# Kernel optimization log

Hardware: AMD Instinct MI355X
Metric: run time of the kernel (lower is better)

The kernel has to match this reference:

```python
import jax, jax.numpy as jnp
import numpy as np

P_EPS = 1e-6            # nn.PairwiseDistance default eps
ALPHA = 0.25
STD_TARGET = 1.0
NUM_COMMUNITIES = 512   # C = number of unique community ids
BIG = 1e30              # masking value for hard-negative min


def setup_inputs() -> dict:
    key = jax.random.key(0)
    k1, k2, k3 = jax.random.split(key, 3)
    B, N, D, C = 1, 100000, 128, NUM_COMMUNITIES
    node_features = jax.random.normal(k1, (B, N, D), dtype=jnp.float32)
    # row 0: a permutation of node indices; row 1: community of that node.
    perm = jax.random.permutation(k2, N).astype(jnp.int32)
    comm_per_node = jnp.concatenate([
        jnp.arange(C, dtype=jnp.int32),  # guarantee every community appears
        jax.random.randint(k3, (N - C,), 0, C, dtype=jnp.int32),
    ])
    community_belong_list = jnp.stack([perm, comm_per_node[perm]])  # [2, N]
    return {"node_features": node_features, "community_belong_list": community_belong_list}


def reference(node_features, community_belong_list):
    B, N, D = node_features.shape
    C = NUM_COMMUNITIES
    dt = node_features.dtype

    # ---- _community_inverse_permute: invert row-0 permutation, reorder columns ----
    perm = community_belong_list[0]
    inv = jnp.zeros((N,), perm.dtype).at[perm].add(jnp.arange(N, dtype=perm.dtype))
    cbl = community_belong_list[:, inv]          # row0 == arange(N) after this
    comm = cbl[1]                                # [N] community id per node
    src = node_features[:, cbl[0], :]            # [B,N,D] gather (identity order)

    # ---- groupby sum / count -> community means ----
    comm_sum = jnp.zeros((B, C, D), dt).at[:, comm, :].add(src)        # [B,C,D]
    counts = jnp.zeros((C,), dt).at[comm].add(jnp.asarray(1.0, dt))   # [C]
    comm_mean = comm_sum / counts[None, :, None]                      # [B,C,D]

    # ---- cdist(node_features, comm_mean, p=2) -> [B,N,C] ----
    x2 = jnp.sum(node_features * node_features, -1)                   # [B,N]
    c2 = jnp.sum(comm_mean * comm_mean, -1)                           # [B,C]
    dots = jnp.einsum('bnd,bcd->bnc', node_features, comm_mean)
    distance = jnp.sqrt(jnp.maximum(x2[:, :, None] + c2[:, None, :] - 2.0 * dots, 0.0))

    # ---- leave-one-out community mean per node, positive distance ----
    cnt_pn = counts[comm]                                             # [N]
    cnt_m1 = jnp.maximum(cnt_pn - 1.0, 1.0)                           # [N]
    x_minus = jnp.where((cnt_pn == 1.0)[None, :, None], jnp.asarray(0.0, dt), src)
    loo_mean = (comm_sum[:, comm, :] - x_minus) / cnt_m1[None, :, None]
    pos_dist = jnp.sqrt(jnp.sum((loo_mean - src + P_EPS) ** 2, -1))   # [B,N]

    # ---- negatives: all communities except the node's own ----
    own = distance[:, jnp.arange(N), comm]                            # [B,N]
    mean_neg = (jnp.sum(distance, -1) - own) / (C - 1)                # [B,N]
    pos_mask = jnp.zeros((N, C), bool).at[jnp.arange(N), comm].set(True)
    hard_neg = jnp.min(jnp.where(pos_mask[None], jnp.asarray(BIG, dt), distance), -1)

    trip_mean = jnp.maximum(pos_dist - mean_neg + ALPHA, 0.0)
    trip_min = jnp.maximum(pos_dist - hard_neg + ALPHA, 0.0)

    # ---- groupby std (unbiased) per community per feature ----
    sq = jnp.zeros((B, C, D), dt).at[:, comm, :].add((src - comm_mean[:, comm, :]) ** 2)
    std = jnp.sqrt(sq / jnp.maximum(counts - 1.0, 1.0)[None, :, None])

    return (trip_mean.mean(), trip_min.mean(), ((std - STD_TARGET) ** 2).mean())
```

## Files before the change

### kernel.cpp

```cpp
#include <hip/hip_runtime.h>

#define NCOMM 512
#define DIM   128
#define ALPHA 0.25f
#define PEPS  1e-6f
#define BIGF  1e30f
#define TILE_C 16
#define NT    (NCOMM / TILE_C)

typedef __attribute__((ext_vector_type(8))) _Float16 f16x8;
typedef __attribute__((ext_vector_type(4))) float f32x4;

#define GLOAD_LDS16(g, l) __builtin_amdgcn_global_load_lds( \
    (const __attribute__((address_space(1))) void*)(g), \
    (__attribute__((address_space(3))) void*)(l), 16, 0, 0)


__global__ void k_prep(const int* __restrict__ cbl, int* __restrict__ comm,
                       int* __restrict__ counts, int N) {
    __shared__ int h[NCOMM];
    int t = threadIdx.x;
    h[t] = 0; h[t + 256] = 0;
    __syncthreads();
    int i = blockIdx.x * 256 + t;
    if (i < N) {
        int p = cbl[i];
        int c = cbl[N + i];
        comm[p] = c;
        atomicAdd(&h[c], 1);
    }
    __syncthreads();
    int v = h[t];        if (v) atomicAdd(&counts[t], v);
    v = h[t + 256];      if (v) atomicAdd(&counts[t + 256], v);
}

__global__ void k_scan(const int* __restrict__ counts, int* __restrict__ offsets,
                       int* __restrict__ cursor, float* __restrict__ countf) {
    __shared__ int sc[NCOMM];
    int t = threadIdx.x;
    int v0 = counts[t];
    sc[t] = v0;
    __syncthreads();
    for (int off = 1; off < NCOMM; off <<= 1) {
        int v = (t >= off) ? sc[t - off] : 0;
        __syncthreads();
        sc[t] += v;
        __syncthreads();
    }
    int excl = sc[t] - v0;
    offsets[t] = excl;
    cursor[t]  = excl;
    countf[t]  = (float)v0;
}

__global__ void k_sort(const int* __restrict__ comm, int* __restrict__ cursor,
                       int* __restrict__ sorted, int N) {
    __shared__ int h[NCOMM], hb[NCOMM];
    int t = threadIdx.x;
    h[t] = 0; h[t + 256] = 0;
    __syncthreads();
    int j0 = blockIdx.x * 1024 + t;
    int cs[4];
    #pragma unroll
    for (int q = 0; q < 4; ++q) {
        int j = j0 + q * 256;
        cs[q] = (j < N) ? comm[j] : -1;
        if (cs[q] >= 0) atomicAdd(&h[cs[q]], 1);
    }
    __syncthreads();
    int v = h[t];        if (v) hb[t] = atomicAdd(&cursor[t], v);
    v = h[t + 256];      if (v) hb[t + 256] = atomicAdd(&cursor[t + 256], v);
    __syncthreads();
    #pragma unroll
    for (int q = 0; q < 4; ++q) {
        int j = j0 + q * 256;
        if (cs[q] >= 0) {
            int p = atomicAdd(&hb[cs[q]], 1);
            sorted[p] = j;
        }
    }
}


__global__ void __launch_bounds__(256) k_stats(
        const float* __restrict__ NF,
        const int* __restrict__ sorted, const int* __restrict__ offsets,
        const int* __restrict__ counts,
        float* __restrict__ comm_sum,
        _Float16* __restrict__ CMh,
        float* __restrict__ c2, float* __restrict__ accum) {
    __shared__ int ridx[512];
    __shared__ float4 bufS[256], bufQ[256];
    int c = blockIdx.x, t = threadIdx.x;
    int d4 = t & 31, r = t >> 5;
    int cnt = counts[c], base = offsets[c];
    const float4* NF4 = (const float4*)NF;

    float4 s4 = make_float4(0.f, 0.f, 0.f, 0.f);
    float4 q4 = make_float4(0.f, 0.f, 0.f, 0.f);
    for (int chunk = 0; chunk < cnt; chunk += 512) {
        int m = min(cnt - chunk, 512);
        for (int i = t; i < m; i += 256) ridx[i] = sorted[base + chunk + i];
        __syncthreads();
        int i = r;
        for (; i + 24 < m; i += 32) {
            int a0 = ridx[i], a1 = ridx[i + 8], a2 = ridx[i + 16], a3 = ridx[i + 24];
            float4 v0 = NF4[(size_t)a0 * 32 + d4];
            float4 v1 = NF4[(size_t)a1 * 32 + d4];
            float4 v2 = NF4[(size_t)a2 * 32 + d4];
            float4 v3 = NF4[(size_t)a3 * 32 + d4];
            s4.x += v0.x; s4.y += v0.y; s4.z += v0.z; s4.w += v0.w;
            q4.x = fmaf(v0.x, v0.x, q4.x); q4.y = fmaf(v0.y, v0.y, q4.y);
            q4.z = fmaf(v0.z, v0.z, q4.z); q4.w = fmaf(v0.w, v0.w, q4.w);
            s4.x += v1.x; s4.y += v1.y; s4.z += v1.z; s4.w += v1.w;
            q4.x = fmaf(v1.x, v1.x, q4.x); q4.y = fmaf(v1.y, v1.y, q4.y);
            q4.z = fmaf(v1.z, v1.z, q4.z); q4.w = fmaf(v1.w, v1.w, q4.w);
            s4.x += v2.x; s4.y += v2.y; s4.z += v2.z; s4.w += v2.w;
            q4.x = fmaf(v2.x, v2.x, q4.x); q4.y = fmaf(v2.y, v2.y, q4.y);
            q4.z = fmaf(v2.z, v2.z, q4.z); q4.w = fmaf(v2.w, v2.w, q4.w);
            s4.x += v3.x; s4.y += v3.y; s4.z += v3.z; s4.w += v3.w;
            q4.x = fmaf(v3.x, v3.x, q4.x); q4.y = fmaf(v3.y, v3.y, q4.y);
            q4.z = fmaf(v3.z, v3.z, q4.z); q4.w = fmaf(v3.w, v3.w, q4.w);
        }
        for (; i < m; i += 8) {
            float4 v = NF4[(size_t)ridx[i] * 32 + d4];
            s4.x += v.x; s4.y += v.y; s4.z += v.z; s4.w += v.w;
            q4.x = fmaf(v.x, v.x, q4.x); q4.y = fmaf(v.y, v.y, q4.y);
            q4.z = fmaf(v.z, v.z, q4.z); q4.w = fmaf(v.w, v.w, q4.w);
        }
        __syncthreads();
    }
    bufS[t] = s4; bufQ[t] = q4;
    __syncthreads();
    if (t < 128) {
        float4 a = bufS[t], b = bufS[t + 128];
        a.x += b.x; a.y += b.y; a.z += b.z; a.w += b.w; bufS[t] = a;
        float4 e = bufQ[t], f = bufQ[t + 128];
        e.x += f.x; e.y += f.y; e.z += f.z; e.w += f.w; bufQ[t] = e;
    }
    __syncthreads();
    if (t < 64) {
        float4 a = bufS[t], b = bufS[t + 64];
        a.x += b.x; a.y += b.y; a.z += b.z; a.w += b.w; bufS[t] = a;
        float4 e = bufQ[t], f = bufQ[t + 64];
        e.x += f.x; e.y += f.y; e.z += f.z; e.w += f.w; bufQ[t] = e;
    }
    __syncthreads();
    if (t < 32) {
        float4 a = bufS[t], b = bufS[t + 32];
        a.x += b.x; a.y += b.y; a.z += b.z; a.w += b.w;
        float4 e = bufQ[t], f = bufQ[t + 32];
        e.x += f.x; e.y += f.y; e.z += f.z; e.w += f.w;
        float sarr[4] = {a.x, a.y, a.z, a.w};
        float qarr[4] = {e.x, e.y, e.z, e.w};
        float cf = (float)cnt;
        float mm = 0.f, ee = 0.f;
        #pragma unroll
        for (int k = 0; k < 4; ++k) {
            int d = t * 4 + k;
            float s = sarr[k];
            comm_sum[c * DIM + d] = s;
            float m = (cnt > 0) ? s / cf : 0.f;
            CMh[c * DIM + d] = (_Float16)m;
            float varn = fmaxf(fmaf(-cf * m, m, qarr[k]), 0.f);
            float stdv = sqrtf(varn / fmaxf(cf - 1.f, 1.f));
            float er = stdv - 1.f;
            mm = fmaf(m, m, mm);
            ee = fmaf(er, er, ee);
        }
        #pragma unroll
        for (int msk = 1; msk < 32; msk <<= 1) {
            mm += __shfl_xor(mm, msk);
            ee += __shfl_xor(ee, msk);
        }
        if (t == 0) {
            c2[c] = mm;
            atomicAdd(&accum[2], ee);
        }
    }
}


__global__ void __launch_bounds__(256, 4) k_main(
        const float* __restrict__ NF,
        const _Float16* __restrict__ CMh,
        const float* __restrict__ comm_sum,
        const float* __restrict__ c2g,
        const float* __restrict__ countf,
        const int* __restrict__ comm,
        float* __restrict__ accum, int N) {
    __shared__ _Float16 Bst[4][4][TILE_C * 64];
    __shared__ float c2s[NCOMM];
    __shared__ int   comms[128];
    __shared__ float x2sh[128];
    __shared__ float sums[128], mins[128];
    __shared__ float red[8];

    int tid = threadIdx.x;
    int w  = tid >> 6;
    int l  = tid & 63;
    int lr = l & 15;
    int lk = l >> 4;
    int n0 = blockIdx.x * 128;

    int off0 = ((l >> 3) << 7) + (((l & 7) ^ ((l >> 3) & 7)) << 3);
    const _Float16* gsrc = CMh + off0;
    auto stage = [&](int ss, int b) {
        const _Float16* g = gsrc + (size_t)(ss >> 1) * 2048 + (ss & 1) * 64;
        _Float16* lh = &Bst[w][b][0];
        GLOAD_LDS16(g,        lh);
        GLOAD_LDS16(g + 1024, lh + 512);
    };
    stage(0, 0); stage(1, 1); stage(2, 2);

    c2s[tid]       = c2g[tid];
    c2s[tid + 256] = c2g[tid + 256];
    if (tid < 128) {
        int gn = n0 + tid;
        comms[tid] = (gn < N) ? comm[gn] : -1;
    }

    f16x8 ah[2][4];
    #pragma unroll
    for (int mf = 0; mf < 2; ++mf) {
        int n = n0 + w * 32 + mf * 16 + lr;
        const float4* src = (const float4*)NF + (size_t)n * 32 + lk * 2;
        float p2 = 0.f;
        #pragma unroll
        for (int ks = 0; ks < 4; ++ks) {
            float4 v0 = make_float4(0.f, 0.f, 0.f, 0.f), v1 = v0;
            if (n < N) { v0 = src[ks * 8]; v1 = src[ks * 8 + 1]; }
            float fr[8] = {v0.x, v0.y, v0.z, v0.w, v1.x, v1.y, v1.z, v1.w};
            f16x8 hh;
            #pragma unroll
            for (int t = 0; t < 8; ++t) {
                hh[t] = (_Float16)fr[t];
                p2 = fmaf(fr[t], fr[t], p2);
            }
            ah[mf][ks] = hh;
        }
        p2 += __shfl_xor(p2, 16);
        p2 += __shfl_xor(p2, 32);
        if (lk == 0) x2sh[w * 32 + mf * 16 + lr] = -0.5f * p2;
    }
    __syncthreads();

    f32x4 x2v[2];
    int cnv[2][4];
    float sumv[2][4], minv[2][4];
    #pragma unroll
    for (int mf = 0; mf < 2; ++mf) {
        x2v[mf] = *(const f32x4*)&x2sh[w * 32 + mf * 16 + lk * 4];
        #pragma unroll
        for (int j = 0; j < 4; ++j) {
            cnv[mf][j] = comms[w * 32 + mf * 16 + lk * 4 + j];
            sumv[mf][j] = 0.f; minv[mf][j] = BIGF;
        }
    }

    for (int tt = 0; tt < NT; ++tt) {
        f32x4 acc0, acc1;
        {
            int ssn = 2 * tt + 3;
            if (ssn < 64) stage(ssn, ssn & 3);
            if (tt <= 30) { asm volatile("s_waitcnt vmcnt(6)" ::: "memory"); }
            else          { asm volatile("s_waitcnt vmcnt(2)" ::: "memory"); }
            const _Float16* bp = &Bst[w][(2 * tt) & 3][0];
            acc0 = x2v[0]; acc1 = x2v[1];
            #pragma unroll
            for (int ks2 = 0; ks2 < 2; ++ks2) {
                int ch = (ks2 * 4 + lk) ^ (lr & 7);
                f16x8 b = *(const f16x8*)&bp[(size_t)(lr * 64 + ch * 8)];
                acc0 = __builtin_amdgcn_mfma_f32_16x16x32_f16(ah[0][ks2], b, acc0, 0, 0, 0);
                acc1 = __builtin_amdgcn_mfma_f32_16x16x32_f16(ah[1][ks2], b, acc1, 0, 0, 0);
            }
        }
        {
            int ssn = 2 * tt + 4;
            if (ssn < 64) stage(ssn, ssn & 3);
            if (tt <= 29)      { asm volatile("s_waitcnt vmcnt(6)" ::: "memory"); }
            else if (tt == 30) { asm volatile("s_waitcnt vmcnt(4)" ::: "memory"); }
            else               { asm volatile("s_waitcnt vmcnt(0)" ::: "memory"); }
            const _Float16* bp = &Bst[w][(2 * tt + 1) & 3][0];
            #pragma unroll
            for (int ks2 = 0; ks2 < 2; ++ks2) {
                int ch = (ks2 * 4 + lk) ^ (lr & 7);
                f16x8 b = *(const f16x8*)&bp[(size_t)(lr * 64 + ch * 8)];
                acc0 = __builtin_amdgcn_mfma_f32_16x16x32_f16(ah[0][2 + ks2], b, acc0, 0, 0, 0);
                acc1 = __builtin_amdgcn_mfma_f32_16x16x32_f16(ah[1][2 + ks2], b, acc1, 0, 0, 0);
            }
            int ccol = tt * TILE_C + lr;
            float c2v = c2s[ccol];
            #pragma unroll
            for (int j = 0; j < 4; ++j) {
                float d2a = fmaf(-2.f, acc0[j], c2v);
                float da  = __builtin_amdgcn_sqrtf(fmaxf(d2a, 0.f));
                sumv[0][j] += da;
                minv[0][j] = fminf(minv[0][j], (cnv[0][j] == ccol) ? BIGF : da);
                float d2b = fmaf(-2.f, acc1[j], c2v);
                float db  = __builtin_amdgcn_sqrtf(fmaxf(d2b, 0.f));
                sumv[1][j] += db;
                minv[1][j] = fminf(minv[1][j], (cnv[1][j] == ccol) ? BIGF : db);
            }
        }
    }

    #pragma unroll
    for (int mf = 0; mf < 2; ++mf)
        #pragma unroll
        for (int j = 0; j < 4; ++j) {
            float sv = sumv[mf][j], mv = minv[mf][j];
            #pragma unroll
            for (int msk = 1; msk < 16; msk <<= 1) {
                sv += __shfl_xor(sv, msk);
                mv = fminf(mv, __shfl_xor(mv, msk));
            }
            if (lr == 0) {
                int idx = w * 32 + mf * 16 + lk * 4 + j;
                sums[idx] = sv; mins[idx] = mv;
            }
        }
    __syncthreads();

    float tmean = 0.f, tminv = 0.f;
    {
        int ln = tid >> 1, half = tid & 1;
        int n = n0 + ln;
        if (n < N) {
            int cnode = comms[ln];
            float cf  = countf[cnode];
            float cm1 = fmaxf(cf - 1.f, 1.f);
            float rs  = 1.f / cm1;
            bool single = (cf == 1.f);
            const float4* srow = (const float4*)NF + (size_t)n * 32 + half * 16;
            const float4* csum = (const float4*)(comm_sum + (size_t)cnode * DIM) + half * 16;
            float q = 0.f, dot = 0.f;
            #pragma unroll
            for (int m = 0; m < 16; ++m) {
                float4 sv = srow[m];
                float4 cs = csum[m];
                float4 xm = single ? make_float4(0.f, 0.f, 0.f, 0.f) : sv;
                float lx = (cs.x - xm.x) * rs - sv.x + PEPS;
                float ly = (cs.y - xm.y) * rs - sv.y + PEPS;
                float lz = (cs.z - xm.z) * rs - sv.z + PEPS;
                float lw = (cs.w - xm.w) * rs - sv.w + PEPS;
                q = fmaf(lx, lx, fmaf(ly, ly, fmaf(lz, lz, fmaf(lw, lw, q))));
                dot = fmaf(sv.x, cs.x, fmaf(sv.y, cs.y, fmaf(sv.z, cs.z, fmaf(sv.w, cs.w, dot))));
            }
            q   += __shfl_xor(q, 1);
            dot += __shfl_xor(dot, 1);
            if (half == 0) {
                float pos = sqrtf(q);
                float x2 = -2.f * x2sh[ln];
                float ownd2 = x2 + c2s[cnode] - 2.f * (dot / cf);
                float own = sqrtf(fmaxf(ownd2, 0.f));
                float mean_neg = (sums[ln] - own) * (1.f / (float)(NCOMM - 1));
                tmean = fmaxf(pos - mean_neg + ALPHA, 0.f);
                tminv = fmaxf(pos - mins[ln] + ALPHA, 0.f);
            }
        }
    }
    #pragma unroll
    for (int msk = 1; msk < 64; msk <<= 1) {
        tmean += __shfl_xor(tmean, msk);
        tminv += __shfl_xor(tminv, msk);
    }
    if ((tid & 63) == 0) { red[w * 2] = tmean; red[w * 2 + 1] = tminv; }
    __syncthreads();
    if (tid == 0) {
        atomicAdd(&accum[0], red[0] + red[2] + red[4] + red[6]);
        atomicAdd(&accum[1], red[1] + red[3] + red[5] + red[7]);
    }
}

__global__ void k_final(const float* __restrict__ accum, float* __restrict__ out, int N) {
    if (threadIdx.x == 0) {
        out[0] = accum[0] / (float)N;
        out[1] = accum[1] / (float)N;
        out[2] = accum[2] / (float)(NCOMM * DIM);
    }
}


extern "C" void kernel_launch(void* const* d_in, const int* in_sizes, int n_in,
                              void* d_out, int out_size, void* d_ws, size_t ws_size,
                              hipStream_t stream) {
    const float* NF  = (const float*)d_in[0];
    const int*   CBL = (const int*)d_in[1];
    int N = in_sizes[1] / 2;
    if (N <= 0) return;

    char* ws = (char*)d_ws;
    float* accum   = (float*)ws;
    int*   counts  = (int*)(ws + 16);
    int*   cursor  = (int*)(ws + 16 + 2048);
    int*   offsets = (int*)(ws + 16 + 2 * 2048);
    float* countf  = (float*)(ws + 16 + 3 * 2048);
    float* c2      = (float*)(ws + 16 + 4 * 2048);
    char* p = ws + 16 + 5 * 2048;
    int* comm   = (int*)p; p += (size_t)N * 4;
    int* sorted = (int*)p; p += (size_t)N * 4;
    float* comm_sum = (float*)p; p += (size_t)NCOMM * DIM * 4;
    _Float16* CMh = (_Float16*)p;

    hipMemsetAsync(d_ws, 0, 16 + 2048, stream);

    int nb = (N + 255) / 256;
    k_prep<<<nb, 256, 0, stream>>>(CBL, comm, counts, N);
    k_scan<<<1, NCOMM, 0, stream>>>(counts, offsets, cursor, countf);
    int nb4 = (N + 1023) / 1024;
    k_sort<<<nb4, 256, 0, stream>>>(comm, cursor, sorted, N);
    k_stats<<<NCOMM, 256, 0, stream>>>(NF, sorted, offsets, counts,
                                       comm_sum, CMh, c2, accum);
    int mb = (N + 127) / 128;
    k_main<<<mb, 256, 0, stream>>>(NF, CMh, comm_sum, c2, countf,
                                   comm, accum, N);
    k_final<<<1, 64, 0, stream>>>(accum, (float*)d_out, N);
}
```

Baseline: 120.8 us.

## Use 2 waves per block with 64 rows each to double B-tile reuse

Result: faster. 118.2 us (median of 2 runs) (-2.2%).

```diff
diff --git a/kernel.cpp b/kernel.cpp
--- a/kernel.cpp
+++ b/kernel.cpp
@@ -181,7 +181,7 @@
 }
 
 
-__global__ void __launch_bounds__(256, 4) k_main(
+__global__ void __launch_bounds__(128, 2) k_main(
         const float* __restrict__ NF,
         const _Float16* __restrict__ CMh,
         const float* __restrict__ comm_sum,
@@ -189,12 +189,12 @@
         const float* __restrict__ countf,
         const int* __restrict__ comm,
         float* __restrict__ accum, int N) {
-    __shared__ _Float16 Bst[4][4][TILE_C * 64];
+    __shared__ _Float16 Bst[2][4][TILE_C * 64];
     __shared__ float c2s[NCOMM];
     __shared__ int   comms[128];
     __shared__ float x2sh[128];
     __shared__ float sums[128], mins[128];
-    __shared__ float red[8];
+    __shared__ float red[4];
 
     int tid = threadIdx.x;
     int w  = tid >> 6;
@@ -214,16 +214,18 @@
     stage(0, 0); stage(1, 1); stage(2, 2);
 
     c2s[tid]       = c2g[tid];
+    c2s[tid + 128] = c2g[tid + 128];
     c2s[tid + 256] = c2g[tid + 256];
-    if (tid < 128) {
+    c2s[tid + 384] = c2g[tid + 384];
+    {
         int gn = n0 + tid;
         comms[tid] = (gn < N) ? comm[gn] : -1;
     }
 
-    f16x8 ah[2][4];
-    #pragma unroll
-    for (int mf = 0; mf < 2; ++mf) {
-        int n = n0 + w * 32 + mf * 16 + lr;
+    f16x8 ah[4][4];
+    #pragma unroll
+    for (int mf = 0; mf < 4; ++mf) {
+        int n = n0 + w * 64 + mf * 16 + lr;
         const float4* src = (const float4*)NF + (size_t)n * 32 + lk * 2;
         float p2 = 0.f;
         #pragma unroll
@@ -241,38 +243,40 @@
         }
         p2 += __shfl_xor(p2, 16);
         p2 += __shfl_xor(p2, 32);
-        if (lk == 0) x2sh[w * 32 + mf * 16 + lr] = -0.5f * p2;
-    }
-    __syncthreads();
-
-    f32x4 x2v[2];
-    int cnv[2][4];
-    float sumv[2][4], minv[2][4];
-    #pragma unroll
-    for (int mf = 0; mf < 2; ++mf) {
-        x2v[mf] = *(const f32x4*)&x2sh[w * 32 + mf * 16 + lk * 4];
+        if (lk == 0) x2sh[w * 64 + mf * 16 + lr] = -0.5f * p2;
+    }
+    __syncthreads();
+
+    f32x4 x2v[4];
+    int cnv[4][4];
+    float sumv[4][4], minv[4][4];
+    #pragma unroll
+    for (int mf = 0; mf < 4; ++mf) {
+        x2v[mf] = *(const f32x4*)&x2sh[w * 64 + mf * 16 + lk * 4];
         #pragma unroll
         for (int j = 0; j < 4; ++j) {
-            cnv[mf][j] = comms[w * 32 + mf * 16 + lk * 4 + j];
+            cnv[mf][j] = comms[w * 64 + mf * 16 + lk * 4 + j];
             sumv[mf][j] = 0.f; minv[mf][j] = BIGF;
         }
     }
 
     for (int tt = 0; tt < NT; ++tt) {
-        f32x4 acc0, acc1;
+        f32x4 acc0, acc1, acc2, acc3;
         {
             int ssn = 2 * tt + 3;
             if (ssn < 64) stage(ssn, ssn & 3);
             if (tt <= 30) { asm volatile("s_waitcnt vmcnt(6)" ::: "memory"); }
             else          { asm volatile("s_waitcnt vmcnt(2)" ::: "memory"); }
             const _Float16* bp = &Bst[w][(2 * tt) & 3][0];
-            acc0 = x2v[0]; acc1 = x2v[1];
+            acc0 = x2v[0]; acc1 = x2v[1]; acc2 = x2v[2]; acc3 = x2v[3];
             #pragma unroll
             for (int ks2 = 0; ks2 < 2; ++ks2) {
                 int ch = (ks2 * 4 + lk) ^ (lr & 7);
                 f16x8 b = *(const f16x8*)&bp[(size_t)(lr * 64 + ch * 8)];
                 acc0 = __builtin_amdgcn_mfma_f32_16x16x32_f16(ah[0][ks2], b, acc0, 0, 0, 0);
                 acc1 = __builtin_amdgcn_mfma_f32_16x16x32_f16(ah[1][ks2], b, acc1, 0, 0, 0);
+                acc2 = __builtin_amdgcn_mfma_f32_16x16x32_f16(ah[2][ks2], b, acc2, 0, 0, 0);
+                acc3 = __builtin_amdgcn_mfma_f32_16x16x32_f16(ah[3][ks2], b, acc3, 0, 0, 0);
             }
         }
         {
@@ -288,6 +292,8 @@
                 f16x8 b = *(const f16x8*)&bp[(size_t)(lr * 64 + ch * 8)];
                 acc0 = __builtin_amdgcn_mfma_f32_16x16x32_f16(ah[0][2 + ks2], b, acc0, 0, 0, 0);
                 acc1 = __builtin_amdgcn_mfma_f32_16x16x32_f16(ah[1][2 + ks2], b, acc1, 0, 0, 0);
+                acc2 = __builtin_amdgcn_mfma_f32_16x16x32_f16(ah[2][2 + ks2], b, acc2, 0, 0, 0);
+                acc3 = __builtin_amdgcn_mfma_f32_16x16x32_f16(ah[3][2 + ks2], b, acc3, 0, 0, 0);
             }
             int ccol = tt * TILE_C + lr;
             float c2v = c2s[ccol];
@@ -301,12 +307,20 @@
                 float db  = __builtin_amdgcn_sqrtf(fmaxf(d2b, 0.f));
                 sumv[1][j] += db;
                 minv[1][j] = fminf(minv[1][j], (cnv[1][j] == ccol) ? BIGF : db);
-            }
-        }
-    }
-
-    #pragma unroll
-    for (int mf = 0; mf < 2; ++mf)
+                float d2c = fmaf(-2.f, acc2[j], c2v);
+                float dc  = __builtin_amdgcn_sqrtf(fmaxf(d2c, 0.f));
+                sumv[2][j] += dc;
+                minv[2][j] = fminf(minv[2][j], (cnv[2][j] == ccol) ? BIGF : dc);
+                float d2d = fmaf(-2.f, acc3[j], c2v);
+                float dd  = __builtin_amdgcn_sqrtf(fmaxf(d2d, 0.f));
+                sumv[3][j] += dd;
+                minv[3][j] = fminf(minv[3][j], (cnv[3][j] == ccol) ? BIGF : dd);
+            }
+        }
+    }
+
+    #pragma unroll
+    for (int mf = 0; mf < 4; ++mf)
         #pragma unroll
         for (int j = 0; j < 4; ++j) {
             float sv = sumv[mf][j], mv = minv[mf][j];
@@ -316,7 +330,7 @@
                 mv = fminf(mv, __shfl_xor(mv, msk));
             }
             if (lr == 0) {
-                int idx = w * 32 + mf * 16 + lk * 4 + j;
+                int idx = w * 64 + mf * 16 + lk * 4 + j;
                 sums[idx] = sv; mins[idx] = mv;
             }
         }
@@ -324,7 +338,7 @@
 
     float tmean = 0.f, tminv = 0.f;
     {
-        int ln = tid >> 1, half = tid & 1;
+        int ln = tid;
         int n = n0 + ln;
         if (n < N) {
             int cnode = comms[ln];
@@ -332,11 +346,11 @@
             float cm1 = fmaxf(cf - 1.f, 1.f);
             float rs  = 1.f / cm1;
             bool single = (cf == 1.f);
-            const float4* srow = (const float4*)NF + (size_t)n * 32 + half * 16;
-            const float4* csum = (const float4*)(comm_sum + (size_t)cnode * DIM) + half * 16;
+            const float4* srow = (const float4*)NF + (size_t)n * 32;
+            const float4* csum = (const float4*)(comm_sum + (size_t)cnode * DIM);
             float q = 0.f, dot = 0.f;
-            #pragma unroll
-            for (int m = 0; m < 16; ++m) {
+            #pragma unroll 8
+            for (int m = 0; m < 32; ++m) {
                 float4 sv = srow[m];
                 float4 cs = csum[m];
                 float4 xm = single ? make_float4(0.f, 0.f, 0.f, 0.f) : sv;
@@ -347,17 +361,13 @@
                 q = fmaf(lx, lx, fmaf(ly, ly, fmaf(lz, lz, fmaf(lw, lw, q))));
                 dot = fmaf(sv.x, cs.x, fmaf(sv.y, cs.y, fmaf(sv.z, cs.z, fmaf(sv.w, cs.w, dot))));
             }
-            q   += __shfl_xor(q, 1);
-            dot += __shfl_xor(dot, 1);
-            if (half == 0) {
-                float pos = sqrtf(q);
-                float x2 = -2.f * x2sh[ln];
-                float ownd2 = x2 + c2s[cnode] - 2.f * (dot / cf);
-                float own = sqrtf(fmaxf(ownd2, 0.f));
-                float mean_neg = (sums[ln] - own) * (1.f / (float)(NCOMM - 1));
-                tmean = fmaxf(pos - mean_neg + ALPHA, 0.f);
-                tminv = fmaxf(pos - mins[ln] + ALPHA, 0.f);
-            }
+            float pos = sqrtf(q);
+            float x2 = -2.f * x2sh[ln];
+            float ownd2 = x2 + c2s[cnode] - 2.f * (dot / cf);
+            float own = sqrtf(fmaxf(ownd2, 0.f));
+            float mean_neg = (sums[ln] - own) * (1.f / (float)(NCOMM - 1));
+            tmean = fmaxf(pos - mean_neg + ALPHA, 0.f);
+            tminv = fmaxf(pos - mins[ln] + ALPHA, 0.f);
         }
     }
     #pragma unroll
@@ -365,11 +375,11 @@
         tmean += __shfl_xor(tmean, msk);
         tminv += __shfl_xor(tminv, msk);
     }
-    if ((tid & 63) == 0) { red[w * 2] = tmean; red[w * 2 + 1] = tminv; }
+    if (l == 0) { red[w * 2] = tmean; red[w * 2 + 1] = tminv; }
     __syncthreads();
     if (tid == 0) {
-        atomicAdd(&accum[0], red[0] + red[2] + red[4] + red[6]);
-        atomicAdd(&accum[1], red[1] + red[3] + red[5] + red[7]);
+        atomicAdd(&accum[0], red[0] + red[2]);
+        atomicAdd(&accum[1], red[1] + red[3]);
     }
 }
 
@@ -413,7 +423,7 @@
     k_stats<<<NCOMM, 256, 0, stream>>>(NF, sorted, offsets, counts,
                                        comm_sum, CMh, c2, accum);
     int mb = (N + 127) / 128;
-    k_main<<<mb, 256, 0, stream>>>(NF, CMh, comm_sum, c2, countf,
+    k_main<<<mb, 128, 0, stream>>>(NF, CMh, comm_sum, c2, countf,
                                    comm, accum, N);
     k_final<<<1, 64, 0, stream>>>(accum, (float*)d_out, N);
 }
```

## Use one wave per block computing 128 rows to share B-tile loads

Applied to the files above, without the earlier changes.

New measurement: 138.8 us. 14.9% more time.

```diff
diff --git a/kernel.cpp b/kernel.cpp
--- a/kernel.cpp
+++ b/kernel.cpp
@@ -181,7 +181,7 @@
 }
 
 
-__global__ void __launch_bounds__(256, 4) k_main(
+__global__ void __launch_bounds__(64, 1) k_main(
         const float* __restrict__ NF,
         const _Float16* __restrict__ CMh,
         const float* __restrict__ comm_sum,
@@ -189,41 +189,40 @@
         const float* __restrict__ countf,
         const int* __restrict__ comm,
         float* __restrict__ accum, int N) {
-    __shared__ _Float16 Bst[4][4][TILE_C * 64];
+    __shared__ _Float16 Bst[4][TILE_C * 64];
     __shared__ float c2s[NCOMM];
     __shared__ int   comms[128];
     __shared__ float x2sh[128];
     __shared__ float sums[128], mins[128];
-    __shared__ float red[8];
 
     int tid = threadIdx.x;
-    int w  = tid >> 6;
-    int l  = tid & 63;
-    int lr = l & 15;
-    int lk = l >> 4;
+    int lr = tid & 15;
+    int lk = tid >> 4;
     int n0 = blockIdx.x * 128;
 
-    int off0 = ((l >> 3) << 7) + (((l & 7) ^ ((l >> 3) & 7)) << 3);
+    int off0 = ((tid >> 3) << 7) + (((tid & 7) ^ ((tid >> 3) & 7)) << 3);
     const _Float16* gsrc = CMh + off0;
     auto stage = [&](int ss, int b) {
         const _Float16* g = gsrc + (size_t)(ss >> 1) * 2048 + (ss & 1) * 64;
-        _Float16* lh = &Bst[w][b][0];
+        _Float16* lh = &Bst[b][0];
         GLOAD_LDS16(g,        lh);
         GLOAD_LDS16(g + 1024, lh + 512);
     };
     stage(0, 0); stage(1, 1); stage(2, 2);
 
-    c2s[tid]       = c2g[tid];
-    c2s[tid + 256] = c2g[tid + 256];
-    if (tid < 128) {
+    #pragma unroll
+    for (int q = 0; q < 8; ++q) c2s[q * 64 + tid] = c2g[q * 64 + tid];
+    {
         int gn = n0 + tid;
         comms[tid] = (gn < N) ? comm[gn] : -1;
-    }
-
-    f16x8 ah[2][4];
-    #pragma unroll
-    for (int mf = 0; mf < 2; ++mf) {
-        int n = n0 + w * 32 + mf * 16 + lr;
+        gn = n0 + 64 + tid;
+        comms[64 + tid] = (gn < N) ? comm[gn] : -1;
+    }
+
+    f16x8 ah[8][4];
+    #pragma unroll
+    for (int mf = 0; mf < 8; ++mf) {
+        int n = n0 + mf * 16 + lr;
         const float4* src = (const float4*)NF + (size_t)n * 32 + lk * 2;
         float p2 = 0.f;
         #pragma unroll
@@ -241,38 +240,40 @@
         }
         p2 += __shfl_xor(p2, 16);
         p2 += __shfl_xor(p2, 32);
-        if (lk == 0) x2sh[w * 32 + mf * 16 + lr] = -0.5f * p2;
-    }
-    __syncthreads();
-
-    f32x4 x2v[2];
-    int cnv[2][4];
-    float sumv[2][4], minv[2][4];
-    #pragma unroll
-    for (int mf = 0; mf < 2; ++mf) {
-        x2v[mf] = *(const f32x4*)&x2sh[w * 32 + mf * 16 + lk * 4];
+        if (lk == 0) x2sh[mf * 16 + lr] = -0.5f * p2;
+    }
+    __syncthreads();
+
+    f32x4 x2v[8];
+    int cnv[8][4];
+    float sumv[8][4], minv[8][4];
+    #pragma unroll
+    for (int mf = 0; mf < 8; ++mf) {
+        x2v[mf] = *(const f32x4*)&x2sh[mf * 16 + lk * 4];
         #pragma unroll
         for (int j = 0; j < 4; ++j) {
-            cnv[mf][j] = comms[w * 32 + mf * 16 + lk * 4 + j];
+            cnv[mf][j] = comms[mf * 16 + lk * 4 + j];
             sumv[mf][j] = 0.f; minv[mf][j] = BIGF;
         }
     }
 
     for (int tt = 0; tt < NT; ++tt) {
-        f32x4 acc0, acc1;
+        f32x4 acc[8];
         {
             int ssn = 2 * tt + 3;
             if (ssn < 64) stage(ssn, ssn & 3);
             if (tt <= 30) { asm volatile("s_waitcnt vmcnt(6)" ::: "memory"); }
             else          { asm volatile("s_waitcnt vmcnt(2)" ::: "memory"); }
-            const _Float16* bp = &Bst[w][(2 * tt) & 3][0];
-            acc0 = x2v[0]; acc1 = x2v[1];
+            const _Float16* bp = &Bst[(2 * tt) & 3][0];
+            #pragma unroll
+            for (int mf = 0; mf < 8; ++mf) acc[mf] = x2v[mf];
             #pragma unroll
             for (int ks2 = 0; ks2 < 2; ++ks2) {
                 int ch = (ks2 * 4 + lk) ^ (lr & 7);
                 f16x8 b = *(const f16x8*)&bp[(size_t)(lr * 64 + ch * 8)];
-                acc0 = __builtin_amdgcn_mfma_f32_16x16x32_f16(ah[0][ks2], b, acc0, 0, 0, 0);
-                acc1 = __builtin_amdgcn_mfma_f32_16x16x32_f16(ah[1][ks2], b, acc1, 0, 0, 0);
+                #pragma unroll
+                for (int mf = 0; mf < 8; ++mf)
+                    acc[mf] = __builtin_amdgcn_mfma_f32_16x16x32_f16(ah[mf][ks2], b, acc[mf], 0, 0, 0);
             }
         }
         {
@@ -281,32 +282,31 @@
             if (tt <= 29)      { asm volatile("s_waitcnt vmcnt(6)" ::: "memory"); }
             else if (tt == 30) { asm volatile("s_waitcnt vmcnt(4)" ::: "memory"); }
             else               { asm volatile("s_waitcnt vmcnt(0)" ::: "memory"); }
-            const _Float16* bp = &Bst[w][(2 * tt + 1) & 3][0];
+            const _Float16* bp = &Bst[(2 * tt + 1) & 3][0];
             #pragma unroll
             for (int ks2 = 0; ks2 < 2; ++ks2) {
                 int ch = (ks2 * 4 + lk) ^ (lr & 7);
                 f16x8 b = *(const f16x8*)&bp[(size_t)(lr * 64 + ch * 8)];
-                acc0 = __builtin_amdgcn_mfma_f32_16x16x32_f16(ah[0][2 + ks2], b, acc0, 0, 0, 0);
-                acc1 = __builtin_amdgcn_mfma_f32_16x16x32_f16(ah[1][2 + ks2], b, acc1, 0, 0, 0);
+                #pragma unroll
+                for (int mf = 0; mf < 8; ++mf)
+                    acc[mf] = __builtin_amdgcn_mfma_f32_16x16x32_f16(ah[mf][2 + ks2], b, acc[mf], 0, 0, 0);
             }
             int ccol = tt * TILE_C + lr;
             float c2v = c2s[ccol];
             #pragma unroll
-            for (int j = 0; j < 4; ++j) {
-                float d2a = fmaf(-2.f, acc0[j], c2v);
-                float da  = __builtin_amdgcn_sqrtf(fmaxf(d2a, 0.f));
-                sumv[0][j] += da;
-                minv[0][j] = fminf(minv[0][j], (cnv[0][j] == ccol) ? BIGF : da);
-                float d2b = fmaf(-2.f, acc1[j], c2v);
-                float db  = __builtin_amdgcn_sqrtf(fmaxf(d2b, 0.f));
-                sumv[1][j] += db;
-                minv[1][j] = fminf(minv[1][j], (cnv[1][j] == ccol) ? BIGF : db);
-            }
-        }
-    }
-
-    #pragma unroll
-    for (int mf = 0; mf < 2; ++mf)
+            for (int mf = 0; mf < 8; ++mf)
+                #pragma unroll
+                for (int j = 0; j < 4; ++j) {
+                    float d2 = fmaf(-2.f, acc[mf][j], c2v);
+                    float da = __builtin_amdgcn_sqrtf(fmaxf(d2, 0.f));
+                    sumv[mf][j] += da;
+                    minv[mf][j] = fminf(minv[mf][j], (cnv[mf][j] == ccol) ? BIGF : da);
+                }
+        }
+    }
+
+    #pragma unroll
+    for (int mf = 0; mf < 8; ++mf)
         #pragma unroll
         for (int j = 0; j < 4; ++j) {
             float sv = sumv[mf][j], mv = minv[mf][j];
@@ -316,15 +316,15 @@
                 mv = fminf(mv, __shfl_xor(mv, msk));
             }
             if (lr == 0) {
-                int idx = w * 32 + mf * 16 + lk * 4 + j;
+                int idx = mf * 16 + lk * 4 + j;
                 sums[idx] = sv; mins[idx] = mv;
             }
         }
     __syncthreads();
 
     float tmean = 0.f, tminv = 0.f;
-    {
-        int ln = tid >> 1, half = tid & 1;
+    for (int rr = 0; rr < 2; ++rr) {
+        int ln = rr * 64 + tid;
         int n = n0 + ln;
         if (n < N) {
             int cnode = comms[ln];
@@ -332,11 +332,11 @@
             float cm1 = fmaxf(cf - 1.f, 1.f);
             float rs  = 1.f / cm1;
             bool single = (cf == 1.f);
-            const float4* srow = (const float4*)NF + (size_t)n * 32 + half * 16;
-            const float4* csum = (const float4*)(comm_sum + (size_t)cnode * DIM) + half * 16;
+            const float4* srow = (const float4*)NF + (size_t)n * 32;
+            const float4* csum = (const float4*)(comm_sum + (size_t)cnode * DIM);
             float q = 0.f, dot = 0.f;
-            #pragma unroll
-            for (int m = 0; m < 16; ++m) {
+            #pragma unroll 8
+            for (int m = 0; m < 32; ++m) {
                 float4 sv = srow[m];
                 float4 cs = csum[m];
                 float4 xm = single ? make_float4(0.f, 0.f, 0.f, 0.f) : sv;
@@ -347,17 +347,13 @@
                 q = fmaf(lx, lx, fmaf(ly, ly, fmaf(lz, lz, fmaf(lw, lw, q))));
                 dot = fmaf(sv.x, cs.x, fmaf(sv.y, cs.y, fmaf(sv.z, cs.z, fmaf(sv.w, cs.w, dot))));
             }
-            q   += __shfl_xor(q, 1);
-            dot += __shfl_xor(dot, 1);
-            if (half == 0) {
-                float pos = sqrtf(q);
-                float x2 = -2.f * x2sh[ln];
-                float ownd2 = x2 + c2s[cnode] - 2.f * (dot / cf);
-                float own = sqrtf(fmaxf(ownd2, 0.f));
-                float mean_neg = (sums[ln] - own) * (1.f / (float)(NCOMM - 1));
-                tmean = fmaxf(pos - mean_neg + ALPHA, 0.f);
-                tminv = fmaxf(pos - mins[ln] + ALPHA, 0.f);
-            }
+            float pos = sqrtf(q);
+            float x2 = -2.f * x2sh[ln];
+            float ownd2 = x2 + c2s[cnode] - 2.f * (dot / cf);
+            float own = sqrtf(fmaxf(ownd2, 0.f));
+            float mean_neg = (sums[ln] - own) * (1.f / (float)(NCOMM - 1));
+            tmean += fmaxf(pos - mean_neg + ALPHA, 0.f);
+            tminv += fmaxf(pos - mins[ln] + ALPHA, 0.f);
         }
     }
     #pragma unroll
@@ -365,11 +361,9 @@
         tmean += __shfl_xor(tmean, msk);
         tminv += __shfl_xor(tminv, msk);
     }
-    if ((tid & 63) == 0) { red[w * 2] = tmean; red[w * 2 + 1] = tminv; }
-    __syncthreads();
     if (tid == 0) {
-        atomicAdd(&accum[0], red[0] + red[2] + red[4] + red[6]);
-        atomicAdd(&accum[1], red[1] + red[3] + red[5] + red[7]);
+        atomicAdd(&accum[0], tmean);
+        atomicAdd(&accum[1], tminv);
     }
 }
 
@@ -413,7 +407,7 @@
     k_stats<<<NCOMM, 256, 0, stream>>>(NF, sorted, offsets, counts,
                                        comm_sum, CMh, c2, accum);
     int mb = (N + 127) / 128;
-    k_main<<<mb, 256, 0, stream>>>(NF, CMh, comm_sum, c2, countf,
-                                   comm, accum, N);
+    k_main<<<mb, 64, 0, stream>>>(NF, CMh, comm_sum, c2, countf,
+                                  comm, accum, N);
     k_final<<<1, 64, 0, stream>>>(accum, (float*)d_out, N);
 }
```
